# Optimization experiments

Measured on AMD Instinct MI355X. Metric: run time of the kernel, lower is better.

Reference implementation:

```python
import jax, jax.numpy as jnp
import numpy as np

N_NODES = 100000
N_EDGES = 3200000
IN_C = 128
HID_C = 128
NUM_LAYERS = 8
ALPHA = 0.1
THETA = 0.5


def setup_inputs() -> dict:
    key = jax.random.key(0)
    kx, ks, kd, kp, kw = jax.random.split(key, 5)
    x = jax.random.normal(kx, (N_NODES, IN_C), dtype=jnp.float32)
    src = jax.random.randint(ks, (N_EDGES,), 0, N_NODES, dtype=jnp.int32)
    dst = jax.random.randint(kd, (N_EDGES,), 0, N_NODES, dtype=jnp.int32)
    dst = jnp.where(src == dst, (dst + 1) % N_NODES, dst)  # no self-loops; gcn_norm adds them
    edge_index = jnp.stack([src, dst])  # [2, E], row=source, col=target
    # proj: Linear(in_c, hid_c)
    W_proj = jax.random.normal(kp, (IN_C, HID_C), dtype=jnp.float32) * (1.0 / np.sqrt(IN_C))
    b_proj = jnp.zeros((HID_C,), dtype=jnp.float32)
    # GCN2Conv weight1 per layer (glorot-ish), shared_weights=True -> single weight
    conv_weights = jax.random.normal(kw, (NUM_LAYERS, HID_C, HID_C), dtype=jnp.float32) * (1.0 / np.sqrt(HID_C))
    return {"x": x, "edge_index": edge_index, "W_proj": W_proj, "b_proj": b_proj, "conv_weights": conv_weights}


def reference(x, edge_index, W_proj, b_proj, conv_weights):
    row, col = edge_index[0], edge_index[1]
    loop = jnp.arange(N_NODES, dtype=row.dtype)
    row_f = jnp.concatenate([row, loop])  # add self-loops (gcn_norm)
    col_f = jnp.concatenate([col, loop])
    deg = jax.ops.segment_sum(jnp.ones(row_f.shape[0], x.dtype), col_f, num_segments=N_NODES)
    dinv = jnp.where(deg > 0, jax.lax.rsqrt(jnp.maximum(deg, 1e-12)), 0.0)
    norm = dinv[row_f] * dinv[col_f]  # [E+N] symmetric GCN normalization

    x0 = x @ W_proj + b_proj  # [N, HID_C]
    h = x0
    betas = np.log(THETA / np.arange(1, NUM_LAYERS + 1) + 1.0)  # beta_l = log(theta/l + 1)
    for i in range(NUM_LAYERS):
        # message passing: gather from source, scale, scatter-add to target
        agg = jax.ops.segment_sum(norm[:, None] * h[row_f], col_f, num_segments=N_NODES)
        z = (1.0 - ALPHA) * agg + ALPHA * x0
        beta = float(betas[i])
        raw = (1.0 - beta) * z + beta * (z @ conv_weights[i])
        h = raw + h  # residual
        if i != NUM_LAYERS - 1:
            h = jax.nn.relu(h)
    return h
```

## Files before the change

kernel.cpp:

```cpp
#include <hip/hip_runtime.h>
#include <cmath>

#define NN 100000
#define NE 3200000
#define C 128
#define NLAYERS 8
#define PSTRIDE 96

#define NBUCK 391
#define EPB 4096
#define NBLK 782
#define SEGCAP 48

typedef unsigned int u32;
typedef unsigned short u16;
typedef __attribute__((ext_vector_type(8))) short s16x8;
typedef __attribute__((ext_vector_type(4))) float f32x4;

__device__ __forceinline__ float bf2f(u16 u) { return __uint_as_float(((u32)u) << 16); }
__device__ __forceinline__ u16 f2bf(float f) {
    u32 x = __float_as_uint(f);
    return (u16)((x + 0x7fffu + ((x >> 16) & 1u)) >> 16);
}


__global__ __launch_bounds__(256) void binpass(
    const int* __restrict__ row, const int* __restrict__ col,
    u32* __restrict__ barr, u32* __restrict__ bcnt) {
    __shared__ u32 hist[NBUCK];
    int tid = threadIdx.x, blk = blockIdx.x;
    for (int i = tid; i < NBUCK; i += 256) hist[i] = 0;
    __syncthreads();
    int e0 = blk * EPB;
    int ee = min(e0 + EPB, NE);
    u32 segbase = (u32)blk * NBUCK * SEGCAP;
    for (int e = e0 + tid; e < ee; e += 256) {
        int d = col[e];
        int s = row[e];
        int b = d >> 8;
        u32 r = atomicAdd(&hist[b], 1u);
        if (r < SEGCAP)
            barr[segbase + (u32)b * SEGCAP + r] = (u32)s | ((u32)(d & 255) << 17);
    }
    __syncthreads();
    for (int i = tid; i < NBUCK; i += 256)
        bcnt[(size_t)i * NBLK + blk] = min(hist[i], (u32)SEGCAP);
}

__global__ __launch_bounds__(1024) void fillpass(
    const u32* __restrict__ barr, const u32* __restrict__ bcnt,
    int* __restrict__ csr, int* __restrict__ cnt, float* __restrict__ dinv) {
    __shared__ u32 counts[NBLK];
    __shared__ u32 lcnt[256];
    int tid = threadIdx.x, b = blockIdx.x;
    for (int i = tid; i < NBLK; i += 1024) counts[i] = bcnt[(size_t)b * NBLK + i];
    if (tid < 256) lcnt[tid] = 0;
    __syncthreads();
    int wave = tid >> 6, lane = tid & 63;
    int nb0 = b << 8;
    int seg = wave;
    u32 c = counts[seg];
    u32 val = (lane < (int)c) ? barr[((u32)seg * NBUCK + b) * SEGCAP + lane] : 0u;
    while (true) {
        int segn = seg + 16;
        u32 cn = 0, valn = 0;
        if (segn < NBLK) {
            cn = counts[segn];
            if (lane < (int)cn) valn = barr[((u32)segn * NBUCK + b) * SEGCAP + lane];
        }
        if (lane < (int)c) {
            int local = (int)(val >> 17);
            u32 slot = atomicAdd(&lcnt[local], 1u);
            csr[(size_t)(nb0 + local) * PSTRIDE + slot] = (int)(val & 0x1FFFFu);
        }
        if (segn >= NBLK) break;
        seg = segn; c = cn; val = valn;
    }
    __syncthreads();
    if (tid < 256 && nb0 + tid < NN) {
        u32 d = lcnt[tid];
        cnt[nb0 + tid] = (int)d;
        dinv[nb0 + tid] = rsqrtf((float)(d + 1));
    }
}

__global__ void prep_w(const float* __restrict__ Wp, const float* __restrict__ cw,
                       u16* __restrict__ Wbh, u16* __restrict__ Wbl) {
    int tid = blockIdx.x * blockDim.x + threadIdx.x;
    if (tid >= 9 * C * C) return;
    int mat = tid >> 14;
    int r = tid & 16383;
    int n = r >> 7, k = r & 127;
    float v;
    if (mat == 0) {
        v = Wp[k * C + n];
    } else {
        float beta = logf(0.5f / (float)mat + 1.0f);
        v = beta * cw[(size_t)(mat - 1) * C * C + k * C + n] +
            ((k == n) ? (1.0f - beta) : 0.0f);
    }
    u16 hi = f2bf(v);
    float lo = v - bf2f(hi);
    Wbh[tid] = hi;
    Wbl[tid] = f2bf(lo);
}


__device__ __forceinline__ void build_a(const float* __restrict__ p, s16x8& hi, s16x8& lo) {
#pragma unroll
    for (int j = 0; j < 8; ++j) {
        float v = p[j];
        u16 h = f2bf(v);
        hi[j] = (short)h;
        lo[j] = (short)f2bf(v - bf2f(h));
    }
}

__global__ __launch_bounds__(256) void gemm_proj(
    const float* __restrict__ X, const u16* __restrict__ Wbh, const u16* __restrict__ Wbl,
    const float* __restrict__ bias, const float* __restrict__ dinv,
    u16* __restrict__ x0bf, float* __restrict__ h32, u16* __restrict__ gbf) {
    int tid = threadIdx.x;
    int wave = tid >> 6, lane = tid & 63;
    int quad = lane >> 4, l16 = lane & 15;
    int rowbase = blockIdx.x * 64 + wave * 16;
    int arow = rowbase + l16;
    if (arow >= NN) arow = NN - 1;
    const float* aptr = X + (size_t)arow * C + quad * 8;
    s16x8 ahi[4], alo[4];
#pragma unroll
    for (int c2 = 0; c2 < 4; ++c2) build_a(aptr + c2 * 32, ahi[c2], alo[c2]);
    f32x4 acc[8];
#pragma unroll
    for (int t = 0; t < 8; ++t) acc[t] = f32x4{0.f, 0.f, 0.f, 0.f};
#pragma unroll
    for (int c2 = 0; c2 < 4; ++c2) {
#pragma unroll
        for (int t = 0; t < 8; ++t) {
            int widx = (t * 16 + l16) * C + c2 * 32 + quad * 8;
            s16x8 bh = *(const s16x8*)(Wbh + widx);
            s16x8 bl = *(const s16x8*)(Wbl + widx);
            acc[t] = __builtin_amdgcn_mfma_f32_16x16x32_bf16(ahi[c2], bh, acc[t], 0, 0, 0);
            acc[t] = __builtin_amdgcn_mfma_f32_16x16x32_bf16(alo[c2], bh, acc[t], 0, 0, 0);
            acc[t] = __builtin_amdgcn_mfma_f32_16x16x32_bf16(ahi[c2], bl, acc[t], 0, 0, 0);
        }
    }
    float dv[4];
#pragma unroll
    for (int r = 0; r < 4; ++r) {
        int m = rowbase + quad * 4 + r;
        dv[r] = (m < NN) ? dinv[m] : 0.f;
    }
#pragma unroll
    for (int t = 0; t < 8; ++t) {
        int n = t * 16 + l16;
        float bv = bias[n];
#pragma unroll
        for (int r = 0; r < 4; ++r) {
            int m = rowbase + quad * 4 + r;
            if (m < NN) {
                float v = acc[t][r] + bv;
                size_t idx = (size_t)m * C + n;
                h32[idx] = v;
                x0bf[idx] = f2bf(v);
                gbf[idx] = f2bf(dv[r] * v);
            }
        }
    }
}


__global__ __launch_bounds__(256) void agg_gemm2(
    const u16* __restrict__ gin, const u16* __restrict__ x0bf,
    const int* __restrict__ cnt, const int* __restrict__ csr,
    const float* __restrict__ dinv,
    const u16* __restrict__ Wbh, const u16* __restrict__ Wbl,
    const float* __restrict__ h32, float* __restrict__ out32,
    u16* __restrict__ gout, int relu) {
    __shared__ u16 zh_lds[16 * C];
    __shared__ u16 zl_lds[16 * C];
    int tid = threadIdx.x;
    int wave = tid >> 6, lane = tid & 63;
    int grp = lane >> 4, l16 = lane & 15;
    int rowbase = blockIdx.x * 16;
    const char* gb = (const char*)gin + l16 * 16;

    float hpre[8];
    float dvr[4];
#pragma unroll
    for (int tt = 0; tt < 2; ++tt) {
        int n = (wave * 2 + tt) * 16 + l16;
#pragma unroll
        for (int r = 0; r < 4; ++r) {
            int m = rowbase + grp * 4 + r;
            hpre[tt * 4 + r] = h32[(size_t)m * C + n];
        }
    }
#pragma unroll
    for (int r = 0; r < 4; ++r) dvr[r] = dinv[rowbase + grp * 4 + r];
    __builtin_amdgcn_sched_barrier(0);

#define ACC8(vv)                                                          \
    {                                                                     \
        u32 x_;                                                           \
        x_ = (u32)(vv).x; a0 += bf2f((u16)x_); a1 += bf2f((u16)(x_ >> 16)); \
        x_ = (u32)(vv).y; a2 += bf2f((u16)x_); a3 += bf2f((u16)(x_ >> 16)); \
        x_ = (u32)(vv).z; a4 += bf2f((u16)x_); a5 += bf2f((u16)(x_ >> 16)); \
        x_ = (u32)(vv).w; a6 += bf2f((u16)x_); a7 += bf2f((u16)(x_ >> 16)); \
    }

    for (int it = 0; it < 4; ++it) {
        int lrow = wave * 4 + it;
        int node = rowbase + lrow;
        int deg = __builtin_amdgcn_readfirstlane(cnt[node]);
        const int* cp = csr + (size_t)node * PSTRIDE;
        float a0 = 0.f, a1 = 0.f, a2 = 0.f, a3 = 0.f, a4 = 0.f, a5 = 0.f, a6 = 0.f, a7 = 0.f;
        int nch = (deg + 15) >> 4;
        if (nch > 0) {
            int dm1 = deg - 1;
            int s0 = cp[min(grp, dm1)];
            int s1 = cp[min(grp + 4, dm1)];
            int s2 = cp[min(grp + 8, dm1)];
            int s3 = cp[min(grp + 12, dm1)];
            for (int c = 0; c < nch; ++c) {
                int4 v0 = *(const int4*)(gb + (size_t)(u32)s0 * 256);
                int4 v1 = *(const int4*)(gb + (size_t)(u32)s1 * 256);
                int4 v2 = *(const int4*)(gb + (size_t)(u32)s2 * 256);
                int4 v3 = *(const int4*)(gb + (size_t)(u32)s3 * 256);
                bool more = (c + 1) < nch;
                if (more) {
                    int nb = (c + 1) << 4;
                    s0 = cp[min(nb + grp, dm1)];
                    s1 = cp[min(nb + grp + 4, dm1)];
                    s2 = cp[min(nb + grp + 8, dm1)];
                    s3 = cp[min(nb + grp + 12, dm1)];
                }
                int cb = c << 4;
                if (cb + 16 <= deg) {
                    ACC8(v0); ACC8(v1); ACC8(v2); ACC8(v3);
                } else {
                    int m0 = (cb + grp < deg) ? -1 : 0;
                    int m1 = (cb + grp + 4 < deg) ? -1 : 0;
                    int m2 = (cb + grp + 8 < deg) ? -1 : 0;
                    int m3 = (cb + grp + 12 < deg) ? -1 : 0;
                    v0.x &= m0; v0.y &= m0; v0.z &= m0; v0.w &= m0;
                    v1.x &= m1; v1.y &= m1; v1.z &= m1; v1.w &= m1;
                    v2.x &= m2; v2.y &= m2; v2.z &= m2; v2.w &= m2;
                    v3.x &= m3; v3.y &= m3; v3.z &= m3; v3.w &= m3;
                    ACC8(v0); ACC8(v1); ACC8(v2); ACC8(v3);
                }
            }
        }
        a0 += __shfl_xor(a0, 16); a0 += __shfl_xor(a0, 32);
        a1 += __shfl_xor(a1, 16); a1 += __shfl_xor(a1, 32);
        a2 += __shfl_xor(a2, 16); a2 += __shfl_xor(a2, 32);
        a3 += __shfl_xor(a3, 16); a3 += __shfl_xor(a3, 32);
        a4 += __shfl_xor(a4, 16); a4 += __shfl_xor(a4, 32);
        a5 += __shfl_xor(a5, 16); a5 += __shfl_xor(a5, 32);
        a6 += __shfl_xor(a6, 16); a6 += __shfl_xor(a6, 32);
        a7 += __shfl_xor(a7, 16); a7 += __shfl_xor(a7, 32);
        int4 sv = *(const int4*)((const char*)gin + (size_t)node * 256 + l16 * 16);
        ACC8(sv);
        float dv = dinv[node];
        int4 xv = *(const int4*)((const char*)x0bf + (size_t)node * 256 + l16 * 16);
        float av[8] = {a0, a1, a2, a3, a4, a5, a6, a7};
        u32 xs[4] = {(u32)xv.x, (u32)xv.y, (u32)xv.z, (u32)xv.w};
        float xf[8];
        xf[0] = bf2f((u16)xs[0]); xf[1] = bf2f((u16)(xs[0] >> 16));
        xf[2] = bf2f((u16)xs[1]); xf[3] = bf2f((u16)(xs[1] >> 16));
        xf[4] = bf2f((u16)xs[2]); xf[5] = bf2f((u16)(xs[2] >> 16));
        xf[6] = bf2f((u16)xs[3]); xf[7] = bf2f((u16)(xs[3] >> 16));
        u32 hp[4], lp[4];
#pragma unroll
        for (int k = 0; k < 4; ++k) {
            float z0 = 0.9f * dv * av[2 * k] + 0.1f * xf[2 * k];
            float z1 = 0.9f * dv * av[2 * k + 1] + 0.1f * xf[2 * k + 1];
            u16 h0 = f2bf(z0), h1 = f2bf(z1);
            u16 l0 = f2bf(z0 - bf2f(h0)), l1 = f2bf(z1 - bf2f(h1));
            hp[k] = (u32)h0 | ((u32)h1 << 16);
            lp[k] = (u32)l0 | ((u32)l1 << 16);
        }
        int bo = (l16 * 16) ^ ((lrow & 7) << 4);
        if (grp == 0) {
            int4 o; o.x = (int)hp[0]; o.y = (int)hp[1]; o.z = (int)hp[2]; o.w = (int)hp[3];
            *(int4*)((char*)zh_lds + lrow * 256 + bo) = o;
        } else if (grp == 1) {
            int4 o; o.x = (int)lp[0]; o.y = (int)lp[1]; o.z = (int)lp[2]; o.w = (int)lp[3];
            *(int4*)((char*)zl_lds + lrow * 256 + bo) = o;
        }
    }
#undef ACC8
    __syncthreads();

    s16x8 ahi[4], alo[4];
#pragma unroll
    for (int c2 = 0; c2 < 4; ++c2) {
        int bo = (c2 * 64 + grp * 16) ^ ((l16 & 7) << 4);
        ahi[c2] = *(const s16x8*)((const char*)zh_lds + l16 * 256 + bo);
        alo[c2] = *(const s16x8*)((const char*)zl_lds + l16 * 256 + bo);
    }
    f32x4 acc[2];
    acc[0] = f32x4{0.f, 0.f, 0.f, 0.f};
    acc[1] = f32x4{0.f, 0.f, 0.f, 0.f};
#pragma unroll
    for (int c2 = 0; c2 < 4; ++c2) {
#pragma unroll
        for (int tt = 0; tt < 2; ++tt) {
            int t = wave * 2 + tt;
            int widx = (t * 16 + l16) * C + c2 * 32 + grp * 8;
            s16x8 bh = *(const s16x8*)(Wbh + widx);
            s16x8 bl = *(const s16x8*)(Wbl + widx);
            acc[tt] = __builtin_amdgcn_mfma_f32_16x16x32_bf16(ahi[c2], bh, acc[tt], 0, 0, 0);
            acc[tt] = __builtin_amdgcn_mfma_f32_16x16x32_bf16(alo[c2], bh, acc[tt], 0, 0, 0);
            acc[tt] = __builtin_amdgcn_mfma_f32_16x16x32_bf16(ahi[c2], bl, acc[tt], 0, 0, 0);
        }
    }
#pragma unroll
    for (int tt = 0; tt < 2; ++tt) {
        int n = (wave * 2 + tt) * 16 + l16;
#pragma unroll
        for (int r = 0; r < 4; ++r) {
            int m = rowbase + grp * 4 + r;
            size_t idx = (size_t)m * C + n;
            float hn = acc[tt][r] + hpre[tt * 4 + r];
            if (relu) hn = fmaxf(hn, 0.f);
            out32[idx] = hn;
            gout[idx] = f2bf(dvr[r] * hn);
        }
    }
}


extern "C" void kernel_launch(void* const* d_in, const int* in_sizes, int n_in,
                              void* d_out, int out_size, void* d_ws, size_t ws_size,
                              hipStream_t stream) {
    const float* x = (const float*)d_in[0];
    const int* ei = (const int*)d_in[1];
    const float* Wp = (const float*)d_in[2];
    const float* bp = (const float*)d_in[3];
    const float* cw = (const float*)d_in[4];
    const int* row = ei;
    const int* col = ei + NE;

    char* ws = (char*)d_ws;
    size_t o = 0;
    auto alloc = [&](size_t bytes) {
        void* p = ws + o;
        o += (bytes + 255) & ~(size_t)255;
        return p;
    };
    int* cnt = (int*)alloc(NN * 4);
    float* dinv = (float*)alloc(NN * 4);
    int* csr = (int*)alloc((size_t)NN * PSTRIDE * 4);
    u16* x0bf = (u16*)alloc((size_t)NN * C * 2);
    u16* gbufA = (u16*)alloc((size_t)NN * C * 2);
    u16* gbufB = (u16*)alloc((size_t)NN * C * 2);
    float* h32 = (float*)alloc((size_t)NN * C * 4);
    u16* Wbh = (u16*)alloc((size_t)9 * C * C * 2);
    u16* Wbl = (u16*)alloc((size_t)9 * C * C * 2);

    char* scratch = (char*)x0bf;
    u32* barr = (u32*)scratch;
    u32* bcnt = (u32*)(scratch + (size_t)NBLK * NBUCK * SEGCAP * 4);

    binpass<<<NBLK, 256, 0, stream>>>(row, col, barr, bcnt);
    fillpass<<<NBUCK, 1024, 0, stream>>>(barr, bcnt, csr, cnt, dinv);
    prep_w<<<(9 * C * C + 255) / 256, 256, 0, stream>>>(Wp, cw, Wbh, Wbl);
    gemm_proj<<<(NN + 63) / 64, 256, 0, stream>>>(x, Wbh, Wbl, bp, dinv, x0bf, h32, gbufA);

    u16* ga = gbufA;
    u16* gb2 = gbufB;
    for (int l = 0; l < NLAYERS; ++l) {
        float* out32 = (l == NLAYERS - 1) ? (float*)d_out : h32;
        agg_gemm2<<<NN / 16, 256, 0, stream>>>(
            ga, x0bf, cnt, csr, dinv,
            Wbh + (size_t)(l + 1) * C * C, Wbl + (size_t)(l + 1) * C * C,
            h32, out32, gb2, (l < NLAYERS - 1) ? 1 : 0);
        u16* tmp = ga; ga = gb2; gb2 = tmp;
    }
}
```

Before: 1.444 ms.

## Fuse all GCN2 layers into one persistent cooperative kernel with grid sync

Replaces the eight per-layer aggregation+GEMM launches with a single persistent cooperative kernel. Each block owns seven 16-row tiles, keeps their fp32 residual state in registers across layers, and uses a grid-wide barrier between layers. This removes the per-layer h32 read/write traffic and the launch overhead, at the cost of grid-sync latency, higher register pressure from holding seven tiles of state, and poorer load balance than a 6250-block launch. A fallback to the per-layer path remains if cooperative launch is unavailable.

```diff
diff --git a/kernel.cpp b/kernel.cpp
--- a/kernel.cpp
+++ b/kernel.cpp
@@ -1,4 +1,5 @@
 #include <hip/hip_runtime.h>
+#include <hip/hip_cooperative_groups.h>
 #include <cmath>
 
 #define NN 100000
@@ -11,6 +12,10 @@
 #define EPB 4096
 #define NBLK 782
 #define SEGCAP 48
+
+#define TPB 7
+#define PGRID 893
+#define NTILE 6250
 
 typedef unsigned int u32;
 typedef unsigned short u16;
@@ -170,36 +175,14 @@
 }
 
 
-__global__ __launch_bounds__(256) void agg_gemm2(
+__device__ __forceinline__ void layer_tile(
+    int rowbase, int wave, int lane, int grp, int l16,
     const u16* __restrict__ gin, const u16* __restrict__ x0bf,
     const int* __restrict__ cnt, const int* __restrict__ csr,
     const float* __restrict__ dinv,
     const u16* __restrict__ Wbh, const u16* __restrict__ Wbl,
-    const float* __restrict__ h32, float* __restrict__ out32,
-    u16* __restrict__ gout, int relu) {
-    __shared__ u16 zh_lds[16 * C];
-    __shared__ u16 zl_lds[16 * C];
-    int tid = threadIdx.x;
-    int wave = tid >> 6, lane = tid & 63;
-    int grp = lane >> 4, l16 = lane & 15;
-    int rowbase = blockIdx.x * 16;
-    const char* gb = (const char*)gin + l16 * 16;
-
-    float hpre[8];
-    float dvr[4];
-#pragma unroll
-    for (int tt = 0; tt < 2; ++tt) {
-        int n = (wave * 2 + tt) * 16 + l16;
-#pragma unroll
-        for (int r = 0; r < 4; ++r) {
-            int m = rowbase + grp * 4 + r;
-            hpre[tt * 4 + r] = h32[(size_t)m * C + n];
-        }
-    }
-#pragma unroll
-    for (int r = 0; r < 4; ++r) dvr[r] = dinv[rowbase + grp * 4 + r];
-    __builtin_amdgcn_sched_barrier(0);
-
+    u16* __restrict__ zh_lds, u16* __restrict__ zl_lds,
+    float* h_reg, float* out32, u16* gout, int relu, int last) {
 #define ACC8(vv)                                                          \
     {                                                                     \
         u32 x_;                                                           \
@@ -208,13 +191,14 @@
         x_ = (u32)(vv).z; a4 += bf2f((u16)x_); a5 += bf2f((u16)(x_ >> 16)); \
         x_ = (u32)(vv).w; a6 += bf2f((u16)x_); a7 += bf2f((u16)(x_ >> 16)); \
     }
-
+    const char* gbp = (const char*)gin + l16 * 16;
     for (int it = 0; it < 4; ++it) {
         int lrow = wave * 4 + it;
         int node = rowbase + lrow;
         int deg = __builtin_amdgcn_readfirstlane(cnt[node]);
         const int* cp = csr + (size_t)node * PSTRIDE;
-        float a0 = 0.f, a1 = 0.f, a2 = 0.f, a3 = 0.f, a4 = 0.f, a5 = 0.f, a6 = 0.f, a7 = 0.f;
+        float a0 = 0.f, a1 = 0.f, a2 = 0.f, a3 = 0.f;
+        float a4 = 0.f, a5 = 0.f, a6 = 0.f, a7 = 0.f;
         int nch = (deg + 15) >> 4;
         if (nch > 0) {
             int dm1 = deg - 1;
@@ -223,10 +207,10 @@
             int s2 = cp[min(grp + 8, dm1)];
             int s3 = cp[min(grp + 12, dm1)];
             for (int c = 0; c < nch; ++c) {
-                int4 v0 = *(const int4*)(gb + (size_t)(u32)s0 * 256);
-                int4 v1 = *(const int4*)(gb + (size_t)(u32)s1 * 256);
-                int4 v2 = *(const int4*)(gb + (size_t)(u32)s2 * 256);
-                int4 v3 = *(const int4*)(gb + (size_t)(u32)s3 * 256);
+                int4 v0 = *(const int4*)(gbp + (size_t)(u32)s0 * 256);
+                int4 v1 = *(const int4*)(gbp + (size_t)(u32)s1 * 256);
+                int4 v2 = *(const int4*)(gbp + (size_t)(u32)s2 * 256);
+                int4 v3 = *(const int4*)(gbp + (size_t)(u32)s3 * 256);
                 bool more = (c + 1) < nch;
                 if (more) {
                     int nb = (c + 1) << 4;
@@ -306,8 +290,8 @@
     for (int c2 = 0; c2 < 4; ++c2) {
 #pragma unroll
         for (int tt = 0; tt < 2; ++tt) {
-            int t = wave * 2 + tt;
-            int widx = (t * 16 + l16) * C + c2 * 32 + grp * 8;
+            int tn = wave * 2 + tt;
+            int widx = (tn * 16 + l16) * C + c2 * 32 + grp * 8;
             s16x8 bh = *(const s16x8*)(Wbh + widx);
             s16x8 bl = *(const s16x8*)(Wbl + widx);
             acc[tt] = __builtin_amdgcn_mfma_f32_16x16x32_bf16(ahi[c2], bh, acc[tt], 0, 0, 0);
@@ -315,6 +299,9 @@
             acc[tt] = __builtin_amdgcn_mfma_f32_16x16x32_bf16(ahi[c2], bl, acc[tt], 0, 0, 0);
         }
     }
+    float dvr[4];
+#pragma unroll
+    for (int r = 0; r < 4; ++r) dvr[r] = dinv[rowbase + grp * 4 + r];
 #pragma unroll
     for (int tt = 0; tt < 2; ++tt) {
         int n = (wave * 2 + tt) * 16 + l16;
@@ -322,10 +309,112 @@
         for (int r = 0; r < 4; ++r) {
             int m = rowbase + grp * 4 + r;
             size_t idx = (size_t)m * C + n;
-            float hn = acc[tt][r] + hpre[tt * 4 + r];
+            float hn = acc[tt][r] + h_reg[tt * 4 + r];
             if (relu) hn = fmaxf(hn, 0.f);
-            out32[idx] = hn;
-            gout[idx] = f2bf(dvr[r] * hn);
+            h_reg[tt * 4 + r] = hn;
+            if (last) {
+                out32[idx] = hn;
+            } else {
+                gout[idx] = f2bf(dvr[r] * hn);
+            }
+        }
+    }
+    __syncthreads();
+}
+
+
+__global__ __launch_bounds__(256, 4) void layers_fused(
+    const u16* __restrict__ ga0, u16* __restrict__ gb0,
+    const u16* __restrict__ x0bf, const int* __restrict__ cnt,
+    const int* __restrict__ csr, const float* __restrict__ dinv,
+    const u16* __restrict__ Wbh0, const u16* __restrict__ Wbl0,
+    const float* __restrict__ h32, float* __restrict__ dout) {
+    __shared__ u16 zh_lds[16 * C];
+    __shared__ u16 zl_lds[16 * C];
+    int tid = threadIdx.x;
+    int wave = tid >> 6, lane = tid & 63;
+    int grp = lane >> 4, l16 = lane & 15;
+    int tile0 = blockIdx.x * TPB;
+
+    float h[TPB][8];
+#pragma unroll
+    for (int t = 0; t < TPB; ++t) {
+        if (tile0 + t >= NTILE) continue;
+        int rowbase = (tile0 + t) * 16;
+#pragma unroll
+        for (int tt = 0; tt < 2; ++tt) {
+            int n = (wave * 2 + tt) * 16 + l16;
+#pragma unroll
+            for (int r = 0; r < 4; ++r)
+                h[t][tt * 4 + r] = h32[(size_t)(rowbase + grp * 4 + r) * C + n];
+        }
+    }
+
+    const u16* gin = ga0;
+    u16* gout = gb0;
+    for (int l = 0; l < NLAYERS; ++l) {
+        const u16* Wbh = Wbh0 + (size_t)(l + 1) * C * C;
+        const u16* Wbl = Wbl0 + (size_t)(l + 1) * C * C;
+        int relu = (l < NLAYERS - 1) ? 1 : 0;
+        int last = (l == NLAYERS - 1) ? 1 : 0;
+#pragma unroll
+        for (int t = 0; t < TPB; ++t) {
+            if (tile0 + t >= NTILE) continue;
+            layer_tile((tile0 + t) * 16, wave, lane, grp, l16,
+                       gin, x0bf, cnt, csr, dinv, Wbh, Wbl,
+                       zh_lds, zl_lds, h[t], dout, gout, relu, last);
+        }
+        if (!last) {
+            __threadfence();
+            cooperative_groups::this_grid().sync();
+            __threadfence();
+            const u16* tmp = gin;
+            gin = gout;
+            gout = (u16*)tmp;
+        }
+    }
+}
+
+
+__global__ __launch_bounds__(256) void agg_gemm2(
+    const u16* __restrict__ gin, const u16* __restrict__ x0bf,
+    const int* __restrict__ cnt, const int* __restrict__ csr,
+    const float* __restrict__ dinv,
+    const u16* __restrict__ Wbh, const u16* __restrict__ Wbl,
+    const float* __restrict__ h32, float* __restrict__ out32,
+    u16* __restrict__ gout, int relu) {
+    __shared__ u16 zh_lds[16 * C];
+    __shared__ u16 zl_lds[16 * C];
+    int tid = threadIdx.x;
+    int wave = tid >> 6, lane = tid & 63;
+    int grp = lane >> 4, l16 = lane & 15;
+    int rowbase = blockIdx.x * 16;
+    float hpre[8];
+#pragma unroll
+    for (int tt = 0; tt < 2; ++tt) {
+        int n = (wave * 2 + tt) * 16 + l16;
+#pragma unroll
+        for (int r = 0; r < 4; ++r)
+            hpre[tt * 4 + r] = h32[(size_t)(rowbase + grp * 4 + r) * C + n];
+    }
+    __builtin_amdgcn_sched_barrier(0);
+    layer_tile(rowbase, wave, lane, grp, l16, gin, x0bf, cnt, csr, dinv,
+               Wbh, Wbl, zh_lds, zl_lds, hpre, out32, gout, relu, 0);
+    if (relu == 0) {
+#pragma unroll
+        for (int tt = 0; tt < 2; ++tt) {
+            int n = (wave * 2 + tt) * 16 + l16;
+#pragma unroll
+            for (int r = 0; r < 4; ++r)
+                out32[(size_t)(rowbase + grp * 4 + r) * C + n] = hpre[tt * 4 + r];
+        }
+    } else {
+#pragma unroll
+        for (int tt = 0; tt < 2; ++tt) {
+            int n = (wave * 2 + tt) * 16 + l16;
+#pragma unroll
+            for (int r = 0; r < 4; ++r)
+                out32[(size_t)(rowbase + grp * 4 + r) * C + n] = hpre[tt * 4 + r];
         }
     }
 }
@@ -368,14 +457,38 @@
     prep_w<<<(9 * C * C + 255) / 256, 256, 0, stream>>>(Wp, cw, Wbh, Wbl);
     gemm_proj<<<(NN + 63) / 64, 256, 0, stream>>>(x, Wbh, Wbl, bp, dinv, x0bf, h32, gbufA);
 
+    static int coopOK = -1;
+    if (coopOK < 0) {
+        int nb = 0;
+        hipError_t e = hipOccupancyMaxActiveBlocksPerMultiprocessor(
+            &nb, layers_fused, 256, 0);
+        int numCU = 0;
+        hipDeviceGetAttribute(&numCU, hipDeviceAttributeMultiprocessorCount, 0);
+        coopOK = (e == hipSuccess && nb > 0 && (long)nb * numCU >= PGRID) ? 1 : 0;
+    }
+
+    if (coopOK) {
+        const u16* ga = gbufA;
+        u16* gb2 = gbufB;
+        float* dout = (float*)d_out;
+        void* args[] = {(void*)&ga, (void*)&gb2, (void*)&x0bf, (void*)&cnt,
+                        (void*)&csr, (void*)&dinv, (void*)&Wbh, (void*)&Wbl,
+                        (void*)&h32, (void*)&dout};
+        hipError_t le = hipLaunchCooperativeKernel((const void*)layers_fused,
+                                                   dim3(PGRID), dim3(256), args,
+                                                   0, stream);
+        if (le == hipSuccess) return;
+        coopOK = 0;
+    }
+
     u16* ga = gbufA;
     u16* gb2 = gbufB;
     for (int l = 0; l < NLAYERS; ++l) {
         float* out32 = (l == NLAYERS - 1) ? (float*)d_out : h32;
-        agg_gemm2<<<NN / 16, 256, 0, stream>>>(
+        agg_gemm2<<<NTILE, 256, 0, stream>>>(
             ga, x0bf, cnt, csr, dinv,
             Wbh + (size_t)(l + 1) * C * C, Wbl + (size_t)(l + 1) * C * C,
-            h32, out32, gb2, (l < NLAYERS - 1) ? 1 : 0);
-        u16* tmp = ga; ga = gb2; gb2 = tmp;
-    }
-}
+            h32, out32, ga == gbufA ? gbufB : gbufA, (l < NLAYERS - 1) ? 1 : 0);
+        u16* tmp = ga; ga = (ga == gbufA) ? gbufB : gbufA; gb2 = tmp;
+    }
+}
```

Result: slower. 1.514 ms (+4.8%).
